# Kernel optimization log

Hardware: AMD Instinct MI355X
Metric: run time of the kernel (lower is better)

The kernel has to match this reference:

```python
import jax, jax.numpy as jnp
import numpy as np

N = 50000
E = 800000
IN_CH = 64
OUT_CH = 64
K = 2  # kernel_size (dim=1, degree=1 B-spline -> linear interpolation)


def setup_inputs() -> dict:
    key = jax.random.key(0)
    k1, k2, k3, k4, k5, k6 = jax.random.split(key, 6)
    x = jax.random.normal(k1, (N, IN_CH), dtype=jnp.float32)
    edge_index = jax.random.randint(k2, (2, E), 0, N, dtype=jnp.int64)
    edge_attr = jax.random.uniform(k3, (E, 1), dtype=jnp.float32)  # pseudo coords in [0,1]
    scale = 1.0 / np.sqrt(IN_CH)
    weight = jax.random.normal(k4, (K, IN_CH, OUT_CH), dtype=jnp.float32) * scale
    root = jax.random.normal(k5, (IN_CH, OUT_CH), dtype=jnp.float32) * scale
    bias = jax.random.normal(k6, (OUT_CH,), dtype=jnp.float32) * 0.01
    return {"x": x, "edge_index": edge_index, "edge_attr": edge_attr,
            "weight": weight, "root": root, "bias": bias}


def reference(x, edge_index, edge_attr, weight, root, bias):
    # SplineConv, dim=1, kernel_size=2, degree=1, open spline, aggr='mean',
    # root_weight=True, bias=True. Followed by ReLU; dropout is identity (eval mode).
    src, dst = edge_index[0], edge_index[1]
    u = edge_attr[:, 0]                      # [E], pseudo in [0,1]
    v = u * (K - 1)
    i0 = jnp.clip(jnp.floor(v).astype(jnp.int32), 0, K - 1)
    i1 = jnp.clip(i0 + 1, 0, K - 1)
    f = v - jnp.floor(v)                     # fractional part -> linear basis (1-f, f)
    # Precompute x @ W_k for each kernel index: [K, N, OUT]
    xw = jnp.einsum('ni,kio->kno', x, weight)
    # Per-edge weighted message: [E, OUT]
    m = (1.0 - f)[:, None] * xw[i0, src] + f[:, None] * xw[i1, src]
    # Mean aggregation at target nodes
    agg = jax.ops.segment_sum(m, dst, num_segments=N)
    cnt = jax.ops.segment_sum(jnp.ones((E,), dtype=x.dtype), dst, num_segments=N)
    out = agg / jnp.maximum(cnt, 1.0)[:, None]
    out = out + x @ root + bias
    return jax.nn.relu(out)
```

## Files before the change

kernel.cpp:

```cpp
#include <hip/hip_runtime.h>
#include <hip/hip_bf16.h>
#include <hip/hip_fp16.h>

#define CH 64
#define BSHIFT 7
#define BINSZ 128
#define BCAP 3072
#define QCAP 1024
#define EPB 4096
#define MAXBINS 400

typedef _Float16 f16x8 __attribute__((ext_vector_type(8)));
typedef float f32x4 __attribute__((ext_vector_type(4)));
typedef float f32x2 __attribute__((ext_vector_type(2)));

__global__ __launch_bounds__(256) void prepw_kernel(
        const float* __restrict__ w,
        const float* __restrict__ root,
        _Float16* __restrict__ WT,
        int* __restrict__ bin_cursor, int n_bins) {
    const int t = threadIdx.x;
    if (blockIdx.x == 0)
        for (int i = t; i < n_bins; i += 256) bin_cursor[i] = 0;
    const int gt = blockIdx.x * 256 + t;
    for (int id = gt; id < 192 * 8; id += 2048) {
        int n = id >> 3, c = id & 7;
        const float* src = (n < 128) ? (w + (n >> 6) * 4096 + (n & 63))
                                     : (root + (n - 128));
        f16x8 v;
#pragma unroll
        for (int j = 0; j < 8; ++j) v[j] = (_Float16)src[(c * 8 + j) * 64];
        *(f16x8*)(WT + n * 64 + c * 8) = v;
    }
}

__device__ __forceinline__ void mfma_body(
        int bb, const float* __restrict__ x, const _Float16* __restrict__ WT,
        const float* __restrict__ bias, unsigned short* __restrict__ xwp,
        __half* __restrict__ base, int n_nodes) {
    const int wave = threadIdx.x >> 6, lane = threadIdx.x & 63;
    const int m0 = bb * 64 + wave * 16;
    const int c = lane & 15, g = lane >> 4;
    int arow = m0 + c; if (arow > n_nodes - 1) arow = n_nodes - 1;
    const float* xr = x + (size_t)arow * CH + g * 8;
    f32x4 v0 = *(const f32x4*)(xr);
    f32x4 v1 = *(const f32x4*)(xr + 4);
    f32x4 v2 = *(const f32x4*)(xr + 32);
    f32x4 v3 = *(const f32x4*)(xr + 36);
    f16x8 a0, a1;
#pragma unroll
    for (int j = 0; j < 4; ++j) {
        a0[j] = (_Float16)v0[j]; a0[4 + j] = (_Float16)v1[j];
        a1[j] = (_Float16)v2[j]; a1[4 + j] = (_Float16)v3[j];
    }
    f32x4 acc[12];
#pragma unroll
    for (int nt = 0; nt < 12; ++nt) acc[nt] = (f32x4){0.f, 0.f, 0.f, 0.f};
#pragma unroll
    for (int nt = 0; nt < 12; ++nt) {
        int n = nt * 16 + c;
        f16x8 b0 = *(const f16x8*)(WT + n * 64 + g * 8);
        f16x8 b1 = *(const f16x8*)(WT + n * 64 + 32 + g * 8);
        acc[nt] = __builtin_amdgcn_mfma_f32_16x16x32_f16(a0, b0, acc[nt], 0, 0, 0);
        acc[nt] = __builtin_amdgcn_mfma_f32_16x16x32_f16(a1, b1, acc[nt], 0, 0, 0);
    }
    float bv[4];
#pragma unroll
    for (int gr = 0; gr < 4; ++gr) bv[gr] = bias[gr * 16 + c];
#pragma unroll
    for (int reg = 0; reg < 4; ++reg) {
        int node = m0 + g * 4 + reg;
        if (node < n_nodes) {
#pragma unroll
            for (int gr = 0; gr < 4; ++gr) {
                int ch = gr * 16 + c;
                int pk = __builtin_amdgcn_cvt_pk_fp8_f32(
                    acc[gr][reg], acc[gr + 4][reg], 0, false);
                xwp[(size_t)node * CH + ch] = (unsigned short)(pk & 0xFFFF);
                base[(size_t)node * CH + ch] = __float2half(acc[gr + 8][reg] + bv[gr]);
            }
        }
    }
}

__global__ __launch_bounds__(256) void fused_kernel(
        const float* __restrict__ x, const _Float16* __restrict__ WT,
        const float* __restrict__ bias,
        const int* __restrict__ ei, const float* __restrict__ ea,
        int* __restrict__ bin_cursor, unsigned int* __restrict__ binned,
        unsigned short* __restrict__ xwp, __half* __restrict__ base,
        int n_nodes, int n_edges, int n_bins, int part_blocks) {
    __shared__ uint2 sh[EPB];
    __shared__ int hist[MAXBINS], bstart[MAXBINS + 1];
    __shared__ int gbase[MAXBINS], lcur[MAXBINS];
    if (blockIdx.x >= part_blocks) {
        mfma_body(blockIdx.x - part_blocks, x, WT, bias, xwp, base, n_nodes);
        return;
    }
    const int t = threadIdx.x;
    for (int i = t; i < n_bins; i += 256) hist[i] = 0;
    __syncthreads();
    const int e0 = blockIdx.x * EPB;
    uint2 rec[EPB / 256];
#pragma unroll
    for (int k = 0; k < EPB / 256; ++k) {
        int e = e0 + k * 256 + t;
        if (e < n_edges) {
            int s = ei[e];
            int d = ei[n_edges + e];
            float u = ea[e];
            float fl = floorf(u);
            int i0 = max(0, min((int)fl, 1));
            int i1 = min(i0 + 1, 1);
            float f = u - fl;
            float a1 = ((i0 == 1) ? (1.f - f) : 0.f) + ((i1 == 1) ? f : 0.f);
            unsigned q = __float2uint_rn(a1 * 255.f);
            unsigned dloc = (unsigned)(d & (BINSZ - 1));
            rec[k] = make_uint2((unsigned)s | (q << 16) | (dloc << 24), (unsigned)d);
            atomicAdd(&hist[d >> BSHIFT], 1);
        } else {
            rec[k] = make_uint2(0u, 0xFFFFFFFFu);
        }
    }
    __syncthreads();
    if (t < 64) {
        int carry = 0;
        for (int b = 0; b < n_bins; b += 64) {
            int i = b + t;
            int v = (i < n_bins) ? hist[i] : 0;
            int incl = v;
#pragma unroll
            for (int off = 1; off < 64; off <<= 1) {
                int nv = __shfl_up(incl, off);
                if (t >= off) incl += nv;
            }
            if (i < n_bins) bstart[i] = incl - v + carry;
            carry += __shfl(incl, 63);
        }
        if (t == 0) bstart[n_bins] = carry;
    }
    __syncthreads();
    for (int i = t; i < n_bins; i += 256) {
        int cnt = hist[i];
        gbase[i] = cnt ? atomicAdd(&bin_cursor[i], cnt) : 0;
        lcur[i] = bstart[i];
    }
    __syncthreads();
#pragma unroll
    for (int k = 0; k < EPB / 256; ++k) {
        if (rec[k].y != 0xFFFFFFFFu) {
            int b = (int)(rec[k].y >> BSHIFT);
            int p = atomicAdd(&lcur[b], 1);
            sh[p] = rec[k];
        }
    }
    __syncthreads();
    int total = bstart[n_bins];
    for (int idx = t; idx < total; idx += 256) {
        uint2 r = sh[idx];
        int b = (int)(r.y >> BSHIFT);
        int loc = gbase[b] + (idx - bstart[b]);
        if (loc < BCAP) binned[(size_t)b * BCAP + loc] = r.x;
    }
}

__global__ __launch_bounds__(256) void gatherQ_kernel(
        const unsigned int* __restrict__ binned,
        const int* __restrict__ bin_count,
        const unsigned int* __restrict__ xw32,
        const __half* __restrict__ base,
        float* __restrict__ out,
        int n_nodes) {
    __shared__ unsigned int raw[BCAP];
    __shared__ unsigned int scsr[QCAP];
    __shared__ int dcnt[32], dbase[32], dcur[32];
    const int bin = blockIdx.x >> 2;
    const int qtr = blockIdx.x & 3;
    const int t = threadIdx.x;
    int cnt = bin_count[bin]; if (cnt > BCAP) cnt = BCAP;
    if (t < 32) dcnt[t] = 0;
    __syncthreads();
    for (int i = t; i < cnt; i += 256) {
        unsigned r = binned[(size_t)bin * BCAP + i];
        raw[i] = r;
        int dl = (int)(r >> 24);
        if ((dl >> 5) == qtr) atomicAdd(&dcnt[dl & 31], 1);
    }
    __syncthreads();
    if (t < 32) {
        int v = dcnt[t];
        int incl = v;
#pragma unroll
        for (int off = 1; off < 32; off <<= 1) {
            int nv = __shfl_up(incl, off);
            if (t >= off) incl += nv;
        }
        dbase[t] = incl - v;
        dcur[t] = incl - v;
    }
    __syncthreads();
    for (int i = t; i < cnt; i += 256) {
        unsigned r = raw[i];
        int dl = (int)(r >> 24);
        if ((dl >> 5) == qtr) {
            int p = atomicAdd(&dcur[dl & 31], 1);
            if (p < QCAP) scsr[p] = r & 0x00FFFFFFu;
        }
    }
    __syncthreads();
    const int wave = t >> 6, lane = t & 63;
    const int cl = lane & 31;
    const int wh = lane >> 5;
    const float qs = 1.f / 255.f;
    for (int dl = wave; dl < 32; dl += 4) {
        int node = (bin << BSHIFT) + (qtr << 5) + dl;
        if (node >= n_nodes) continue;
        int deg = dcnt[dl];
        int beg = dbase[dl], end = beg + deg;
        if (end > QCAP) { end = QCAP; deg = end - beg; if (deg < 0) deg = 0; }
        int jend = beg + (deg & ~1);
        float acc0 = 0.f, acc1 = 0.f;
        int j = beg;
        for (; j + 4 <= jend; j += 4) {
            unsigned pA = scsr[j + wh];
            unsigned pB = scsr[j + 2 + wh];
            float uA = (float)((pA >> 16) & 255u) * qs;
            float uB = (float)((pB >> 16) & 255u) * qs;
            unsigned kA = xw32[(size_t)(pA & 0xFFFF) * 32 + cl];
            unsigned kB = xw32[(size_t)(pB & 0xFFFF) * 32 + cl];
            f32x2 a0 = __builtin_amdgcn_cvt_pk_f32_fp8((int)kA, false);
            f32x2 a1 = __builtin_amdgcn_cvt_pk_f32_fp8((int)kA, true);
            f32x2 b0 = __builtin_amdgcn_cvt_pk_f32_fp8((int)kB, false);
            f32x2 b1 = __builtin_amdgcn_cvt_pk_f32_fp8((int)kB, true);
            acc0 += fmaf(uA, a0[1] - a0[0], a0[0]);
            acc1 += fmaf(uA, a1[1] - a1[0], a1[0]);
            acc0 += fmaf(uB, b0[1] - b0[0], b0[0]);
            acc1 += fmaf(uB, b1[1] - b1[0], b1[0]);
        }
        if (j < jend) {
            unsigned pA = scsr[j + wh];
            float uA = (float)((pA >> 16) & 255u) * qs;
            unsigned kA = xw32[(size_t)(pA & 0xFFFF) * 32 + cl];
            f32x2 a0 = __builtin_amdgcn_cvt_pk_f32_fp8((int)kA, false);
            f32x2 a1 = __builtin_amdgcn_cvt_pk_f32_fp8((int)kA, true);
            acc0 += fmaf(uA, a0[1] - a0[0], a0[0]);
            acc1 += fmaf(uA, a1[1] - a1[0], a1[0]);
        }
        if (deg & 1) {
            unsigned pA = scsr[jend];
            float uA = (float)((pA >> 16) & 255u) * qs;
            unsigned kA = xw32[(size_t)(pA & 0xFFFF) * 32 + cl];
            f32x2 a0 = __builtin_amdgcn_cvt_pk_f32_fp8((int)kA, false);
            f32x2 a1 = __builtin_amdgcn_cvt_pk_f32_fp8((int)kA, true);
            if (wh == 0) {
                acc0 += fmaf(uA, a0[1] - a0[0], a0[0]);
                acc1 += fmaf(uA, a1[1] - a1[0], a1[0]);
            }
        }
        acc0 += __shfl_xor(acc0, 32);
        acc1 += __shfl_xor(acc1, 32);
        if (lane < 32) {
            float c = (float)(deg > 0 ? deg : 1);
            size_t o = (size_t)node * CH + 2 * cl;
            __half2 bv = *(const __half2*)(base + o);
            float2 ob;
            ob.x = fmaxf(acc0 / c + __half2float(bv.x), 0.f);
            ob.y = fmaxf(acc1 / c + __half2float(bv.y), 0.f);
            *(float2*)(out + o) = ob;
        }
    }
}

extern "C" void kernel_launch(void* const* d_in, const int* in_sizes, int n_in,
                              void* d_out, int out_size, void* d_ws, size_t ws_size,
                              hipStream_t stream) {
    const float* x    = (const float*)d_in[0];
    const int*   ei   = (const int*)d_in[1];
    const float* ea   = (const float*)d_in[2];
    const float* w    = (const float*)d_in[3];
    const float* root = (const float*)d_in[4];
    const float* bias = (const float*)d_in[5];
    float* out = (float*)d_out;

    const int n_nodes = in_sizes[0] / CH;
    const int n_edges = in_sizes[2];
    const int n_bins  = (n_nodes + BINSZ - 1) >> BSHIFT;
    const int part_blocks = (n_edges + EPB - 1) / EPB;
    const int mfma_blocks = (n_nodes + 63) / 64;

    unsigned short* xwp  = (unsigned short*)d_ws;
    __half*       base   = (__half*)(xwp + (size_t)n_nodes * CH);
    unsigned int* binned = (unsigned int*)(base + (size_t)n_nodes * CH);
    _Float16*     WT     = (_Float16*)(binned + (size_t)n_bins * BCAP);
    int*          bin_cursor = (int*)(WT + 192 * 64);

    prepw_kernel<<<8, 256, 0, stream>>>(w, root, WT, bin_cursor, n_bins);
    fused_kernel<<<part_blocks + mfma_blocks, 256, 0, stream>>>(
        x, WT, bias, ei, ea, bin_cursor, binned, xwp, base,
        n_nodes, n_edges, n_bins, part_blocks);
    gatherQ_kernel<<<4 * n_bins, 256, 0, stream>>>(
        binned, bin_cursor, (const unsigned int*)xwp, base, out, n_nodes);
}
```

Baseline: 64.95 us.

## Split packed xw table into channel halves and run two gather passes

```diff
diff --git a/kernel.cpp b/kernel.cpp
--- a/kernel.cpp
+++ b/kernel.cpp
@@ -36,7 +36,8 @@
 
 __device__ __forceinline__ void mfma_body(
         int bb, const float* __restrict__ x, const _Float16* __restrict__ WT,
-        const float* __restrict__ bias, unsigned short* __restrict__ xwp,
+        const float* __restrict__ bias,
+        unsigned short* __restrict__ xwA, unsigned short* __restrict__ xwB,
         __half* __restrict__ base, int n_nodes) {
     const int wave = threadIdx.x >> 6, lane = threadIdx.x & 63;
     const int m0 = bb * 64 + wave * 16;
@@ -76,7 +77,9 @@
                 int ch = gr * 16 + c;
                 int pk = __builtin_amdgcn_cvt_pk_fp8_f32(
                     acc[gr][reg], acc[gr + 4][reg], 0, false);
-                xwp[(size_t)node * CH + ch] = (unsigned short)(pk & 0xFFFF);
+                unsigned short pv = (unsigned short)(pk & 0xFFFF);
+                if (gr < 2) xwA[(size_t)node * 32 + ch] = pv;
+                else        xwB[(size_t)node * 32 + ch - 32] = pv;
                 base[(size_t)node * CH + ch] = __float2half(acc[gr + 8][reg] + bv[gr]);
             }
         }
@@ -88,13 +91,14 @@
         const float* __restrict__ bias,
         const int* __restrict__ ei, const float* __restrict__ ea,
         int* __restrict__ bin_cursor, unsigned int* __restrict__ binned,
-        unsigned short* __restrict__ xwp, __half* __restrict__ base,
+        unsigned short* __restrict__ xwA, unsigned short* __restrict__ xwB,
+        __half* __restrict__ base,
         int n_nodes, int n_edges, int n_bins, int part_blocks) {
     __shared__ uint2 sh[EPB];
     __shared__ int hist[MAXBINS], bstart[MAXBINS + 1];
     __shared__ int gbase[MAXBINS], lcur[MAXBINS];
     if (blockIdx.x >= part_blocks) {
-        mfma_body(blockIdx.x - part_blocks, x, WT, bias, xwp, base, n_nodes);
+        mfma_body(blockIdx.x - part_blocks, x, WT, bias, xwA, xwB, base, n_nodes);
         return;
     }
     const int t = threadIdx.x;
@@ -164,13 +168,13 @@
     }
 }
 
-__global__ __launch_bounds__(256) void gatherQ_kernel(
+__global__ __launch_bounds__(256) void gatherH_kernel(
         const unsigned int* __restrict__ binned,
         const int* __restrict__ bin_count,
-        const unsigned int* __restrict__ xw32,
+        const unsigned int* __restrict__ xwh,
         const __half* __restrict__ base,
         float* __restrict__ out,
-        int n_nodes) {
+        int n_nodes, int half) {
     __shared__ unsigned int raw[BCAP];
     __shared__ unsigned int scsr[QCAP];
     __shared__ int dcnt[32], dbase[32], dcur[32];
@@ -209,8 +213,8 @@
     }
     __syncthreads();
     const int wave = t >> 6, lane = t & 63;
-    const int cl = lane & 31;
-    const int wh = lane >> 5;
+    const int es = lane >> 4;
+    const int cp = lane & 15;
     const float qs = 1.f / 255.f;
     for (int dl = wave; dl < 32; dl += 4) {
         int node = (bin << BSHIFT) + (qtr << 5) + dl;
@@ -218,16 +222,16 @@
         int deg = dcnt[dl];
         int beg = dbase[dl], end = beg + deg;
         if (end > QCAP) { end = QCAP; deg = end - beg; if (deg < 0) deg = 0; }
-        int jend = beg + (deg & ~1);
         float acc0 = 0.f, acc1 = 0.f;
-        int j = beg;
-        for (; j + 4 <= jend; j += 4) {
-            unsigned pA = scsr[j + wh];
-            unsigned pB = scsr[j + 2 + wh];
+        int tb = beg;
+        int jend = beg + ((end - beg) & ~7);
+        for (; tb < jend; tb += 8) {
+            unsigned pA = scsr[tb + es];
+            unsigned pB = scsr[tb + 4 + es];
             float uA = (float)((pA >> 16) & 255u) * qs;
             float uB = (float)((pB >> 16) & 255u) * qs;
-            unsigned kA = xw32[(size_t)(pA & 0xFFFF) * 32 + cl];
-            unsigned kB = xw32[(size_t)(pB & 0xFFFF) * 32 + cl];
+            unsigned kA = xwh[(size_t)(pA & 0xFFFF) * 16 + cp];
+            unsigned kB = xwh[(size_t)(pB & 0xFFFF) * 16 + cp];
             f32x2 a0 = __builtin_amdgcn_cvt_pk_f32_fp8((int)kA, false);
             f32x2 a1 = __builtin_amdgcn_cvt_pk_f32_fp8((int)kA, true);
             f32x2 b0 = __builtin_amdgcn_cvt_pk_f32_fp8((int)kB, false);
@@ -237,35 +241,27 @@
             acc0 += fmaf(uB, b0[1] - b0[0], b0[0]);
             acc1 += fmaf(uB, b1[1] - b1[0], b1[0]);
         }
-        if (j < jend) {
-            unsigned pA = scsr[j + wh];
-            float uA = (float)((pA >> 16) & 255u) * qs;
-            unsigned kA = xw32[(size_t)(pA & 0xFFFF) * 32 + cl];
-            f32x2 a0 = __builtin_amdgcn_cvt_pk_f32_fp8((int)kA, false);
-            f32x2 a1 = __builtin_amdgcn_cvt_pk_f32_fp8((int)kA, true);
-            acc0 += fmaf(uA, a0[1] - a0[0], a0[0]);
-            acc1 += fmaf(uA, a1[1] - a1[0], a1[0]);
-        }
-        if (deg & 1) {
-            unsigned pA = scsr[jend];
-            float uA = (float)((pA >> 16) & 255u) * qs;
-            unsigned kA = xw32[(size_t)(pA & 0xFFFF) * 32 + cl];
-            f32x2 a0 = __builtin_amdgcn_cvt_pk_f32_fp8((int)kA, false);
-            f32x2 a1 = __builtin_amdgcn_cvt_pk_f32_fp8((int)kA, true);
-            if (wh == 0) {
-                acc0 += fmaf(uA, a0[1] - a0[0], a0[0]);
-                acc1 += fmaf(uA, a1[1] - a1[0], a1[0]);
-            }
-        }
-        acc0 += __shfl_xor(acc0, 32);
-        acc1 += __shfl_xor(acc1, 32);
-        if (lane < 32) {
+        for (; tb < end; tb += 4) {
+            int idx = tb + es;
+            bool v = idx < end;
+            unsigned p = scsr[v ? idx : beg];
+            float u = (float)((p >> 16) & 255u) * qs;
+            float m = v ? 1.f : 0.f;
+            unsigned k = xwh[(size_t)(p & 0xFFFF) * 16 + cp];
+            f32x2 a0 = __builtin_amdgcn_cvt_pk_f32_fp8((int)k, false);
+            f32x2 a1 = __builtin_amdgcn_cvt_pk_f32_fp8((int)k, true);
+            acc0 += m * fmaf(u, a0[1] - a0[0], a0[0]);
+            acc1 += m * fmaf(u, a1[1] - a1[0], a1[0]);
+        }
+        acc0 += __shfl_xor(acc0, 16); acc0 += __shfl_xor(acc0, 32);
+        acc1 += __shfl_xor(acc1, 16); acc1 += __shfl_xor(acc1, 32);
+        if (lane < 16) {
             float c = (float)(deg > 0 ? deg : 1);
-            size_t o = (size_t)node * CH + 2 * cl;
-            __half2 bv = *(const __half2*)(base + o);
+            size_t o = (size_t)node * CH + half * 32 + 2 * cp;
+            float2 bv = __half22float2(*(const __half2*)(base + o));
             float2 ob;
-            ob.x = fmaxf(acc0 / c + __half2float(bv.x), 0.f);
-            ob.y = fmaxf(acc1 / c + __half2float(bv.y), 0.f);
+            ob.x = fmaxf(acc0 / c + bv.x, 0.f);
+            ob.y = fmaxf(acc1 / c + bv.y, 0.f);
             *(float2*)(out + o) = ob;
         }
     }
@@ -288,16 +284,19 @@
     const int part_blocks = (n_edges + EPB - 1) / EPB;
     const int mfma_blocks = (n_nodes + 63) / 64;
 
-    unsigned short* xwp  = (unsigned short*)d_ws;
-    __half*       base   = (__half*)(xwp + (size_t)n_nodes * CH);
+    unsigned short* xwA  = (unsigned short*)d_ws;
+    unsigned short* xwB  = xwA + (size_t)n_nodes * 32;
+    __half*       base   = (__half*)(xwB + (size_t)n_nodes * 32);
     unsigned int* binned = (unsigned int*)(base + (size_t)n_nodes * CH);
     _Float16*     WT     = (_Float16*)(binned + (size_t)n_bins * BCAP);
     int*          bin_cursor = (int*)(WT + 192 * 64);
 
     prepw_kernel<<<8, 256, 0, stream>>>(w, root, WT, bin_cursor, n_bins);
     fused_kernel<<<part_blocks + mfma_blocks, 256, 0, stream>>>(
-        x, WT, bias, ei, ea, bin_cursor, binned, xwp, base,
+        x, WT, bias, ei, ea, bin_cursor, binned, xwA, xwB, base,
         n_nodes, n_edges, n_bins, part_blocks);
-    gatherQ_kernel<<<4 * n_bins, 256, 0, stream>>>(
-        binned, bin_cursor, (const unsigned int*)xwp, base, out, n_nodes);
-}
+    gatherH_kernel<<<4 * n_bins, 256, 0, stream>>>(
+        binned, bin_cursor, (const unsigned int*)xwA, base, out, n_nodes, 0);
+    gatherH_kernel<<<4 * n_bins, 256, 0, stream>>>(
+        binned, bin_cursor, (const unsigned int*)xwB, base, out, n_nodes, 1);
+}
```

Measured after the change: 79.77 us. 22.8% more time.
